# Kernel tuning notes

Hardware: AMD Instinct MI355X
Metric: run time of the kernel (lower is better)

Reference implementation:

```python
import jax, jax.numpy as jnp
import numpy as np

B, N, F = 8, 2048, 32  # batch, num_nodes, out_features
AVG_DEG = 32


def setup_inputs() -> dict:
    key = jax.random.key(0)
    k1, k2, k3, k4 = jax.random.split(key, 4)
    x = jax.random.normal(k1, (B, N, N + 1), dtype=jnp.float32)
    # kaiming-uniform-ish scale for weight, small uniform for bias
    bound_w = 1.0 / np.sqrt(N + 1)
    weight = jax.random.uniform(k2, (N, N + 1, F), jnp.float32, -bound_w, bound_w)
    bound_b = 1.0 / np.sqrt((N + 1) * F)
    bias = jax.random.uniform(k3, (N, F), jnp.float32, -bound_b, bound_b)
    # random symmetric adjacency with self-loops, avg degree ~AVG_DEG
    adj = jax.random.bernoulli(k4, AVG_DEG / N, (N, N))
    adj = adj | adj.T | jnp.eye(N, dtype=bool)
    # prepend an always-kept column (the ones column in the torch code)
    keep = jnp.concatenate([jnp.ones((N, 1), dtype=bool), adj], axis=1)  # [N, N+1]
    edge_mask = ~keep  # True = zero out (masked_fill semantics)
    return {"x": x, "weight": weight, "bias": bias, "edge_mask": edge_mask}


def reference(x, weight, bias, edge_mask):
    # mask: zero non-neighbor entries per node (broadcast over batch)
    xm = jnp.where(edge_mask[None, :, :], jnp.float32(0.0), x)  # [B, N, N+1]
    # per-node batched matmul: [B,N,N+1] x [N,N+1,F] -> [B,N,F]
    out = jnp.einsum('bnk,nkf->bnf', xm, weight)
    return out + bias[None, :, :]
```

## Files before the change

### kernel.cpp

```cpp
#include <hip/hip_runtime.h>


constexpr int NB = 8;
constexpr int NN = 2048;
constexpr int NK = 2049;
constexpr int NF = 32;
constexpr int BK = 256;
constexpr int NTL = 8;
constexpr size_t XSTR = (size_t)NN * NK;

using f4 = __attribute__((ext_vector_type(4))) float;

__device__ __forceinline__ float ld_scale(const void* __restrict__ mask,
                                          size_t idx, int mode) {
  bool drop;
  if (mode == 0)
    drop = ((const int*)mask)[idx] != 0;
  else if (mode == 1)
    drop = ((const unsigned char*)mask)[idx] != 0;
  else
    drop = ((const float*)mask)[idx] != 0.0f;
  return drop ? 0.0f : 1.0f;
}

__global__ __launch_bounds__(256) void snl_kernel(
    const float* __restrict__ x, const float* __restrict__ w,
    const float* __restrict__ bias, const void* __restrict__ mask,
    float* __restrict__ out) {
  __shared__ float xs[2][NB][BK];
  __shared__ float part[4][8][32];
  __shared__ int smode;

  const int tid = threadIdx.x;
  const int n = blockIdx.x;

  if (tid < 64) {
    unsigned v = ((const unsigned*)mask)[tid];
    unsigned long long bf = __ballot((v >> 24) == 0x3Fu);
    unsigned long long bg = __ballot(v > 1u);
    if (tid == 0) smode = bf ? 2 : (bg ? 1 : 0);
  }
  __syncthreads();
  const int mode = smode;

  const int fq = tid & 7;
  const int kk = (tid >> 3) & 7;
  const int ws = tid >> 6;
  const int lane = tid & 63;
  const int skl = ws * 64 + lane;

  const float* xn = x + (size_t)n * NK;
  const float* wrow = w + (size_t)n * NK * NF;
  const size_t mbase = (size_t)n * NK;

  float acc[NB][4];
#pragma unroll
  for (int b = 0; b < NB; ++b)
#pragma unroll
    for (int j = 0; j < 4; ++j) acc[b][j] = 0.0f;

  {
    const float sc = ld_scale(mask, mbase + skl, mode);
#pragma unroll
    for (int i = 0; i < NB; ++i)
      xs[0][i][skl] =
          __builtin_nontemporal_load(&xn[(size_t)i * XSTR + skl]) * sc;
  }
  __syncthreads();

  for (int t = 0; t < NTL; ++t) {
    const int cur = t & 1;
    const bool pf = (t + 1 < NTL);
    float xr[NB], scr = 0.0f;
    if (pf) {
      const int kg = (t + 1) * BK + skl;
      scr = ld_scale(mask, mbase + kg, mode);
#pragma unroll
      for (int i = 0; i < NB; ++i)
        xr[i] = __builtin_nontemporal_load(&xn[(size_t)i * XSTR + kg]);
    }

    const float* wt = wrow + (size_t)t * BK * NF + (size_t)ws * 64 * NF;
    f4 wv[8];
#pragma unroll
    for (int u = 0; u < 8; ++u)
      wv[u] = __builtin_nontemporal_load(
          (const f4*)(wt + (size_t)(u * 8 + kk) * NF + fq * 4));

#pragma unroll
    for (int u = 0; u < 8; ++u) {
      const int kl = ws * 64 + u * 8 + kk;
#pragma unroll
      for (int b = 0; b < NB; ++b) {
        const float xv = xs[cur][b][kl];
        acc[b][0] = fmaf(xv, wv[u][0], acc[b][0]);
        acc[b][1] = fmaf(xv, wv[u][1], acc[b][1]);
        acc[b][2] = fmaf(xv, wv[u][2], acc[b][2]);
        acc[b][3] = fmaf(xv, wv[u][3], acc[b][3]);
      }
    }

    if (pf) {
#pragma unroll
      for (int i = 0; i < NB; ++i) xs[cur ^ 1][i][skl] = xr[i] * scr;
    }
    __syncthreads();
  }

#pragma unroll
  for (int m = 8; m <= 32; m <<= 1) {
#pragma unroll
    for (int b = 0; b < NB; ++b)
#pragma unroll
      for (int j = 0; j < 4; ++j)
        acc[b][j] += __shfl_xor(acc[b][j], m, 64);
  }
  if (lane < 8) {
#pragma unroll
    for (int b = 0; b < NB; ++b)
#pragma unroll
      for (int j = 0; j < 4; ++j) part[ws][fq][b * 4 + j] = acc[b][j];
  }
  __syncthreads();

  if (tid < 64) {
    const int b = tid >> 3;
    const int f2 = tid & 7;
    f4 o = *(const f4*)(bias + (size_t)n * NF + f2 * 4);
    {
      const float sc = ld_scale(mask, mbase + 2048, mode);
      const float xv = xn[(size_t)b * XSTR + 2048] * sc;
      const f4 wv = *(const f4*)(wrow + (size_t)2048 * NF + f2 * 4);
      o += xv * wv;
    }
#pragma unroll
    for (int wsi = 0; wsi < 4; ++wsi) {
      const f4 p = *(const f4*)&part[wsi][f2][b * 4];
      o += p;
    }
    *(f4*)(out + ((size_t)b * NN + n) * NF + f2 * 4) = o;
  }
}

extern "C" void kernel_launch(void* const* d_in, const int* in_sizes, int n_in,
                              void* d_out, int out_size, void* d_ws,
                              size_t ws_size, hipStream_t stream) {
  const float* x = (const float*)d_in[0];
  const float* w = (const float*)d_in[1];
  const float* bias = (const float*)d_in[2];
  const void* mask = d_in[3];
  float* out = (float*)d_out;

  hipLaunchKernelGGL(snl_kernel, dim3(NN), dim3(256), 0, stream, x, w, bias,
                     mask, out);
}
```

Baseline: 121.9 us.

## Give each wave a contiguous K range and double-buffer weight registers

Each wave now owns a contiguous 512-wide K slice and walks it in 64-row tiles, instead of all waves sharing one 256-wide tile. Weight vectors are kept in two register sets (A/B), so the loads for the next tile are issued before the FMAs on the current one, overlapping memory latency with compute. Barriers are replaced with explicit lgkmcnt waits plus s_barrier and sched_barrier. Holding twice the weight registers raises register pressure and may lower occupancy.

```diff
diff --git a/kernel.cpp b/kernel.cpp
--- a/kernel.cpp
+++ b/kernel.cpp
@@ -5,8 +5,6 @@
 constexpr int NN = 2048;
 constexpr int NK = 2049;
 constexpr int NF = 32;
-constexpr int BK = 256;
-constexpr int NTL = 8;
 constexpr size_t XSTR = (size_t)NN * NK;
 
 using f4 = __attribute__((ext_vector_type(4))) float;
@@ -23,11 +21,45 @@
   return drop ? 0.0f : 1.0f;
 }
 
+#define ISSUE_W(dst, t)                                                       \
+  _Pragma("unroll") for (int u = 0; u < 8; ++u) dst[u] =                      \
+      __builtin_nontemporal_load(                                             \
+          (const f4*)(wws + (size_t)((t)*64 + u * 8 + kk) * NF + fq * 4));
+
+#define DO_FMA(src, cur)                                                      \
+  _Pragma("unroll") for (int u = 0; u < 8; ++u) {                             \
+    const int kl = ws * 64 + u * 8 + kk;                                      \
+    _Pragma("unroll") for (int b = 0; b < NB; ++b) {                          \
+      const float xv = xs[cur][b][kl];                                        \
+      acc[b][0] = fmaf(xv, src[u][0], acc[b][0]);                             \
+      acc[b][1] = fmaf(xv, src[u][1], acc[b][1]);                             \
+      acc[b][2] = fmaf(xv, src[u][2], acc[b][2]);                             \
+      acc[b][3] = fmaf(xv, src[u][3], acc[b][3]);                             \
+    }                                                                         \
+  }
+
+#define X_PREFETCH(t)                                                         \
+  {                                                                           \
+    const size_t kg = (size_t)KW + (t)*64 + lane;                             \
+    scr = ld_scale(mask, mbase + kg, mode);                                   \
+    _Pragma("unroll") for (int i = 0; i < NB; ++i) xr[i] =                    \
+        __builtin_nontemporal_load(&xn[(size_t)i * XSTR + kg]);               \
+  }
+
+#define X_WRITE(buf)                                                          \
+  _Pragma("unroll") for (int i = 0; i < NB; ++i) xs[buf][i][ws * 64 + lane] = \
+      xr[i] * scr;
+
+#define TILE_BARRIER()                                  \
+  asm volatile("s_waitcnt lgkmcnt(0)" ::: "memory");    \
+  __builtin_amdgcn_s_barrier();                         \
+  __builtin_amdgcn_sched_barrier(0);
+
 __global__ __launch_bounds__(256) void snl_kernel(
     const float* __restrict__ x, const float* __restrict__ w,
     const float* __restrict__ bias, const void* __restrict__ mask,
     float* __restrict__ out) {
-  __shared__ float xs[2][NB][BK];
+  __shared__ float xs[2][NB][256];
   __shared__ float part[4][8][32];
   __shared__ int smode;
 
@@ -47,10 +79,11 @@
   const int kk = (tid >> 3) & 7;
   const int ws = tid >> 6;
   const int lane = tid & 63;
-  const int skl = ws * 64 + lane;
+  const int KW = ws * 512;
 
   const float* xn = x + (size_t)n * NK;
   const float* wrow = w + (size_t)n * NK * NF;
+  const float* wws = wrow + (size_t)KW * NF;
   const size_t mbase = (size_t)n * NK;
 
   float acc[NB][4];
@@ -59,52 +92,29 @@
 #pragma unroll
     for (int j = 0; j < 4; ++j) acc[b][j] = 0.0f;
 
-  {
-    const float sc = ld_scale(mask, mbase + skl, mode);
-#pragma unroll
-    for (int i = 0; i < NB; ++i)
-      xs[0][i][skl] =
-          __builtin_nontemporal_load(&xn[(size_t)i * XSTR + skl]) * sc;
-  }
-  __syncthreads();
+  f4 wvA[8], wvB[8];
+  float xr[NB], scr;
 
-  for (int t = 0; t < NTL; ++t) {
-    const int cur = t & 1;
-    const bool pf = (t + 1 < NTL);
-    float xr[NB], scr = 0.0f;
-    if (pf) {
-      const int kg = (t + 1) * BK + skl;
-      scr = ld_scale(mask, mbase + kg, mode);
-#pragma unroll
-      for (int i = 0; i < NB; ++i)
-        xr[i] = __builtin_nontemporal_load(&xn[(size_t)i * XSTR + kg]);
+  ISSUE_W(wvA, 0);
+  X_PREFETCH(0);
+  X_WRITE(0);
+  TILE_BARRIER();
+
+  for (int t = 0; t < 8; t += 2) {
+    ISSUE_W(wvB, t + 1);
+    X_PREFETCH(t + 1);
+    DO_FMA(wvA, 0);
+    X_WRITE(1);
+    TILE_BARRIER();
+    if (t + 2 < 8) {
+      ISSUE_W(wvA, t + 2);
+      X_PREFETCH(t + 2);
+      DO_FMA(wvB, 1);
+      X_WRITE(0);
+      TILE_BARRIER();
+    } else {
+      DO_FMA(wvB, 1);
     }
-
-    const float* wt = wrow + (size_t)t * BK * NF + (size_t)ws * 64 * NF;
-    f4 wv[8];
-#pragma unroll
-    for (int u = 0; u < 8; ++u)
-      wv[u] = __builtin_nontemporal_load(
-          (const f4*)(wt + (size_t)(u * 8 + kk) * NF + fq * 4));
-
-#pragma unroll
-    for (int u = 0; u < 8; ++u) {
-      const int kl = ws * 64 + u * 8 + kk;
-#pragma unroll
-      for (int b = 0; b < NB; ++b) {
-        const float xv = xs[cur][b][kl];
-        acc[b][0] = fmaf(xv, wv[u][0], acc[b][0]);
-        acc[b][1] = fmaf(xv, wv[u][1], acc[b][1]);
-        acc[b][2] = fmaf(xv, wv[u][2], acc[b][2]);
-        acc[b][3] = fmaf(xv, wv[u][3], acc[b][3]);
-      }
-    }
-
-    if (pf) {
-#pragma unroll
-      for (int i = 0; i < NB; ++i) xs[cur ^ 1][i][skl] = xr[i] * scr;
-    }
-    __syncthreads();
   }
 
 #pragma unroll
@@ -115,6 +125,7 @@
       for (int j = 0; j < 4; ++j)
         acc[b][j] += __shfl_xor(acc[b][j], m, 64);
   }
+  __syncthreads();
   if (lane < 8) {
 #pragma unroll
     for (int b = 0; b < NB; ++b)
```

Result: no change. 123.5 us (+1.3%).
